# Kernel tuning notes

Measured on AMD Instinct MI355X. Metric: run time of the kernel, lower is better.

## Reference

```python
import jax, jax.numpy as jnp
import numpy as np

B, S, D = 2, 4096, 768
H = 12
HD = D // H  # 64


def setup_inputs() -> dict:
    key = jax.random.key(0)
    ks = jax.random.split(key, 6)
    scale = 0.02
    return {
        "x": jax.random.normal(ks[0], (B, S, D), dtype=jnp.float32),
        "w_query": jax.random.normal(ks[1], (D, D), dtype=jnp.float32) * scale,
        "w_key": jax.random.normal(ks[2], (D, D), dtype=jnp.float32) * scale,
        "w_value": jax.random.normal(ks[3], (D, D), dtype=jnp.float32) * scale,
        "w_out": jax.random.normal(ks[4], (D, D), dtype=jnp.float32) * scale,
        "b_out": jax.random.normal(ks[5], (D,), dtype=jnp.float32) * scale,
    }


def reference(x, w_query, w_key, w_value, w_out, b_out):
    b, s, d = x.shape
    # Linear(in, out) applies x @ W.T; weights here stored as [out, in]-equivalent
    # square matrices, so use x @ W.T for parity with torch semantics.
    q = (x @ w_query.T).reshape(b, s, H, HD).transpose(0, 2, 1, 3)  # [b,h,s,hd]
    k = (x @ w_key.T).reshape(b, s, H, HD).transpose(0, 2, 1, 3)
    v = (x @ w_value.T).reshape(b, s, H, HD).transpose(0, 2, 1, 3)

    scores = jnp.einsum("bhqd,bhkd->bhqk", q, k)  # [b,h,s,s]
    causal = jnp.triu(jnp.ones((s, s), dtype=bool), k=1)
    scores = jnp.where(causal, -jnp.inf, scores)
    # original scales AFTER masking: softmax(masked / sqrt(head_dim))
    att = jax.nn.softmax(scores / jnp.sqrt(jnp.float32(HD)), axis=-1)
    # dropout p=0.0 (eval) -> identity
    ctx = jnp.einsum("bhqk,bhkd->bhqd", att, v)  # [b,h,s,hd]
    ctx = ctx.transpose(0, 2, 1, 3).reshape(b, s, d)
    return ctx @ w_out.T + b_out
```

## Files before the change

### kernel.cpp

```cpp
#include <hip/hip_runtime.h>
#include <stdint.h>

typedef unsigned short u16;
typedef __attribute__((ext_vector_type(8))) short bf16x8;
typedef __attribute__((ext_vector_type(4))) float f32x4;

#define MFMA(a,b,c) __builtin_amdgcn_mfma_f32_16x16x32_bf16((a),(b),(c),0,0,0)

static constexpr int S  = 4096;
static constexpr int D  = 768;
static constexpr int H  = 12;
static constexpr int HD = 64;

__device__ __forceinline__ u16 f2b(float f){
  union { float f; unsigned u; } v; v.f = f;
  unsigned r = (v.u + 0x7fffu + ((v.u >> 16) & 1u)) >> 16;
  return (u16)r;
}

__device__ __forceinline__ unsigned pack_bf16_trunc(float a, float b){
  return __builtin_amdgcn_perm(__float_as_uint(b), __float_as_uint(a), 0x07060302u);
}

__device__ __forceinline__ void cp16(const u16* g, u16* l){
  __builtin_amdgcn_global_load_lds(
      (const __attribute__((address_space(1))) unsigned int*)g,
      (__attribute__((address_space(3))) unsigned int*)l, 16, 0, 0);
}

static constexpr int NX4 = (2 * S * D) / 4;
static constexpr int NW4 = (D * D) / 4;
__global__ void castall(const float* __restrict__ x,  const float* __restrict__ wq,
                        const float* __restrict__ wk, const float* __restrict__ wv,
                        const float* __restrict__ wo,
                        u16* __restrict__ xb,  u16* __restrict__ wqb,
                        u16* __restrict__ wkb, u16* __restrict__ wvb,
                        u16* __restrict__ wob){
  int i = blockIdx.x * 256 + threadIdx.x;
  const float* s; u16* d; int off;
  if (i < NX4) { s = x; d = xb; off = i; }
  else {
    int j = i - NX4; int wsel = j / NW4; off = j - wsel * NW4;
    if (wsel >= 4) return;
    s = (wsel == 0) ? wq : (wsel == 1) ? wk : (wsel == 2) ? wv : wo;
    d = (wsel == 0) ? wqb : (wsel == 1) ? wkb : (wsel == 2) ? wvb : wob;
  }
  float4 v = ((const float4*)s)[off];
  uint2 o;
  o.x = (unsigned)f2b(v.x) | ((unsigned)f2b(v.y) << 16);
  o.y = (unsigned)f2b(v.z) | ((unsigned)f2b(v.w) << 16);
  ((uint2*)d)[off] = o;
}

__global__ __launch_bounds__(256, 2) void qkv_gemm(
    const u16* __restrict__ xb, const u16* __restrict__ wq, const u16* __restrict__ wk,
    const u16* __restrict__ wv, u16* __restrict__ Qb, u16* __restrict__ Kb, u16* __restrict__ Vt)
{
  __shared__ __align__(16) u16 As[128 * 64];
  __shared__ __align__(16) u16 Bs[128 * 64];
  const int t = threadIdx.x;
  const int mblk = blockIdx.x, nblk = blockIdx.y, z = blockIdx.z;
  const u16* W = (z == 0) ? wq : (z == 1) ? wk : wv;
  const int w = t >> 6, lane = t & 63, quad = lane >> 4, l16 = lane & 15;
  const int wr = w >> 1, wc = w & 1;
  const int l7 = l16 & 7;

  f32x4 acc[4][4];
  #pragma unroll
  for (int i = 0; i < 4; i++)
    #pragma unroll
    for (int j = 0; j < 4; j++) acc[i][j] = (f32x4){0.f, 0.f, 0.f, 0.f};

  int srow[4], schk[4];
  #pragma unroll
  for (int i = 0; i < 4; i++) {
    int s = i * 256 + t;
    srow[i] = s >> 3;
    schk[i] = (s & 7) ^ (srow[i] & 7);
  }
  const u16* gA = xb + (size_t)(mblk * 128) * D;
  const u16* gB = W  + (size_t)(nblk * 128) * D;

  for (int k0 = 0; k0 < D; k0 += 64) {
    __syncthreads();
    #pragma unroll
    for (int i = 0; i < 4; i++) {
      int s = i * 256 + t;
      cp16(gA + (size_t)srow[i] * D + k0 + schk[i] * 8, As + s * 8);
      cp16(gB + (size_t)srow[i] * D + k0 + schk[i] * 8, Bs + s * 8);
    }
    __syncthreads();
    #pragma unroll
    for (int j = 0; j < 2; j++) {
      bf16x8 af[4], bfr[4];
      #pragma unroll
      for (int mt = 0; mt < 4; mt++)
        af[mt]  = *(const bf16x8*)(As + (wr * 64 + mt * 16 + l16) * 64 + ((j * 4 + quad) ^ l7) * 8);
      #pragma unroll
      for (int nt = 0; nt < 4; nt++)
        bfr[nt] = *(const bf16x8*)(Bs + (wc * 64 + nt * 16 + l16) * 64 + ((j * 4 + quad) ^ l7) * 8);
      #pragma unroll
      for (int mt = 0; mt < 4; mt++)
        #pragma unroll
        for (int nt = 0; nt < 4; nt++)
          acc[mt][nt] = MFMA(af[mt], bfr[nt], acc[mt][nt]);
    }
  }

  const float qscale = 0.18033688011112042f;
  #pragma unroll
  for (int mt = 0; mt < 4; mt++) {
    int m0 = mblk * 128 + wr * 64 + mt * 16 + quad * 4;
    #pragma unroll
    for (int nt = 0; nt < 4; nt++) {
      int n = nblk * 128 + wc * 64 + nt * 16 + l16;
      int h = n >> 6, hd = n & 63;
      if (z == 2) {
        int b = m0 >> 12, s0 = m0 & 4095;
        u16* p = Vt + (((size_t)(b * H + h) * HD + hd)) * S + s0;
        uint2 pk;
        pk.x = (unsigned)f2b(acc[mt][nt][0]) | ((unsigned)f2b(acc[mt][nt][1]) << 16);
        pk.y = (unsigned)f2b(acc[mt][nt][2]) | ((unsigned)f2b(acc[mt][nt][3]) << 16);
        *(uint2*)p = pk;
      } else {
        u16* dst = (z == 0) ? Qb : Kb;
        float sc = (z == 0) ? qscale : 1.0f;
        #pragma unroll
        for (int r = 0; r < 4; r++) {
          int m = m0 + r; int b = m >> 12, s = m & 4095;
          dst[((size_t)(b * H + h) * S + s) * HD + hd] = f2b(acc[mt][nt][r] * sc);
        }
      }
    }
  }
}

__global__ __launch_bounds__(256, 3) void attn(
    const u16* __restrict__ Qb, const u16* __restrict__ Kb,
    const u16* __restrict__ Vt, u16* __restrict__ ctx)
{
  __shared__ __align__(16) u16 Ks[128 * 64];
  __shared__ __align__(16) u16 Vts[64 * 128];
  __shared__ __align__(16) u16 Pb[4][32 * 72];
  const int t = threadIdx.x, w = t >> 6, lane = t & 63, quad = lane >> 4, l16 = lane & 15;
  const int l7 = l16 & 7;
  const int bh = blockIdx.x;
  const int qtile = 31 - (int)blockIdx.y;
  const int q0 = qtile * 128;
  const u16* Qh = Qb + (size_t)bh * S * HD;
  const u16* Kh = Kb + (size_t)bh * S * HD;
  const u16* Vh = Vt + (size_t)bh * S * HD;
  u16* Pw = &Pb[w][0];
  const int b = bh / H, h = bh % H;

  bf16x8 qf[2][2];
  #pragma unroll
  for (int rt = 0; rt < 2; rt++)
    #pragma unroll
    for (int ks = 0; ks < 2; ks++)
      qf[rt][ks] = *(const bf16x8*)(Qh + (size_t)(q0 + w * 32 + rt * 16 + l16) * HD + ks * 32 + quad * 8);

  f32x4 ao[2][4];
  #pragma unroll
  for (int rt = 0; rt < 2; rt++)
    #pragma unroll
    for (int co = 0; co < 4; co++) ao[rt][co] = (f32x4){0.f, 0.f, 0.f, 0.f};
  float lsum[2] = {0.f, 0.f};

  int krow[4], kchk[4], vrow[4], vchk[4];
  #pragma unroll
  for (int i = 0; i < 4; i++) {
    int s = i * 256 + t;
    krow[i] = s >> 3;  kchk[i] = (s & 7)  ^ (krow[i] & 7);
    vrow[i] = s >> 4;  vchk[i] = (s & 15) ^ (vrow[i] & 15);
  }

  for (int kv0 = 0; kv0 <= q0; kv0 += 128) {
    const bool diag = (kv0 == q0);
    const int ct_end = diag ? (2 * w + 2) : 8;
    const int ks_end = diag ? (w + 1) : 4;

    __syncthreads();
    #pragma unroll
    for (int i = 0; i < 4; i++) {
      int s = i * 256 + t;
      cp16(Kh + (size_t)(kv0 + krow[i]) * HD + kchk[i] * 8, Ks + s * 8);
      cp16(Vh + (size_t)vrow[i] * S + kv0 + vchk[i] * 8,    Vts + s * 8);
    }
    __syncthreads();

    #pragma unroll
    for (int h2 = 0; h2 < 2; h2++) {
      if (h2 * 4 < ct_end) {
        #pragma unroll
        for (int c2 = 0; c2 < 4; c2++) {
          int ct = h2 * 4 + c2;
          if (ct < ct_end) {
            int krw = ct * 16 + l16;
            bf16x8 kf0 = *(const bf16x8*)(Ks + krw * 64 + ((0 + quad) ^ l7) * 8);
            bf16x8 kf1 = *(const bf16x8*)(Ks + krw * 64 + ((4 + quad) ^ l7) * 8);
            f32x4 s0 = (f32x4){0.f, 0.f, 0.f, 0.f};
            f32x4 s1 = (f32x4){0.f, 0.f, 0.f, 0.f};
            s0 = MFMA(kf0, qf[0][0], s0);  s0 = MFMA(kf1, qf[0][1], s0);
            s1 = MFMA(kf0, qf[1][0], s1);  s1 = MFMA(kf1, qf[1][1], s1);
            if (diag) {
              int keyb = kv0 + ct * 16 + quad * 4;
              int qr0  = q0 + w * 32 + l16;
              #pragma unroll
              for (int r = 0; r < 4; r++) {
                if (keyb + r > qr0)      s0[r] = -1e30f;
                if (keyb + r > qr0 + 16) s1[r] = -1e30f;
              }
            }
            float p0 = __builtin_amdgcn_exp2f(s0[0]);
            float p1 = __builtin_amdgcn_exp2f(s0[1]);
            float p2 = __builtin_amdgcn_exp2f(s0[2]);
            float p3 = __builtin_amdgcn_exp2f(s0[3]);
            lsum[0] += (p0 + p1) + (p2 + p3);
            uint2 pk;
            pk.x = pack_bf16_trunc(p0, p1);
            pk.y = pack_bf16_trunc(p2, p3);
            *(uint2*)(Pw + l16 * 72 + c2 * 16 + quad * 4) = pk;
            p0 = __builtin_amdgcn_exp2f(s1[0]);
            p1 = __builtin_amdgcn_exp2f(s1[1]);
            p2 = __builtin_amdgcn_exp2f(s1[2]);
            p3 = __builtin_amdgcn_exp2f(s1[3]);
            lsum[1] += (p0 + p1) + (p2 + p3);
            pk.x = pack_bf16_trunc(p0, p1);
            pk.y = pack_bf16_trunc(p2, p3);
            *(uint2*)(Pw + (16 + l16) * 72 + c2 * 16 + quad * 4) = pk;
          }
        }
        #pragma unroll
        for (int k2 = 0; k2 < 2; k2++) {
          int ks = h2 * 2 + k2;
          if (ks < ks_end) {
            bf16x8 pf0 = *(const bf16x8*)(Pw + (0  + l16) * 72 + k2 * 32 + quad * 8);
            bf16x8 pf1 = *(const bf16x8*)(Pw + (16 + l16) * 72 + k2 * 32 + quad * 8);
            #pragma unroll
            for (int co = 0; co < 4; co++) {
              int vrw = co * 16 + l16;
              bf16x8 vf = *(const bf16x8*)(Vts + vrw * 128 + ((ks * 4 + quad) ^ (vrw & 15)) * 8);
              ao[0][co] = MFMA(vf, pf0, ao[0][co]);
              ao[1][co] = MFMA(vf, pf1, ao[1][co]);
            }
          }
        }
      }
    }
  }

  #pragma unroll
  for (int rt = 0; rt < 2; rt++) {
    float v = lsum[rt];
    v += __shfl_xor(v, 16, 64);
    v += __shfl_xor(v, 32, 64);
    float inv = 1.0f / v;
    int token = b * S + q0 + w * 32 + rt * 16 + l16;
    #pragma unroll
    for (int co = 0; co < 4; co++) {
      uint2 pk;
      pk.x = (unsigned)f2b(ao[rt][co][0] * inv) | ((unsigned)f2b(ao[rt][co][1] * inv) << 16);
      pk.y = (unsigned)f2b(ao[rt][co][2] * inv) | ((unsigned)f2b(ao[rt][co][3] * inv) << 16);
      *(uint2*)(ctx + (size_t)token * D + h * HD + co * 16 + quad * 4) = pk;
    }
  }
}

__global__ __launch_bounds__(256, 2) void out_gemm(
    const u16* __restrict__ ctx, const u16* __restrict__ wo,
    const float* __restrict__ bias, float* __restrict__ out)
{
  __shared__ __align__(16) u16 As[128 * 64];
  __shared__ __align__(16) u16 Bs[128 * 64];
  const int t = threadIdx.x;
  const int mblk = blockIdx.x, nblk = blockIdx.y;
  const int w = t >> 6, lane = t & 63, quad = lane >> 4, l16 = lane & 15;
  const int wr = w >> 1, wc = w & 1;
  const int l7 = l16 & 7;

  f32x4 acc[4][4];
  #pragma unroll
  for (int i = 0; i < 4; i++)
    #pragma unroll
    for (int j = 0; j < 4; j++) acc[i][j] = (f32x4){0.f, 0.f, 0.f, 0.f};

  int srow[4], schk[4];
  #pragma unroll
  for (int i = 0; i < 4; i++) {
    int s = i * 256 + t;
    srow[i] = s >> 3;
    schk[i] = (s & 7) ^ (srow[i] & 7);
  }
  const u16* gA = ctx + (size_t)(mblk * 128) * D;
  const u16* gB = wo  + (size_t)(nblk * 128) * D;

  for (int k0 = 0; k0 < D; k0 += 64) {
    __syncthreads();
    #pragma unroll
    for (int i = 0; i < 4; i++) {
      int s = i * 256 + t;
      cp16(gA + (size_t)srow[i] * D + k0 + schk[i] * 8, As + s * 8);
      cp16(gB + (size_t)srow[i] * D + k0 + schk[i] * 8, Bs + s * 8);
    }
    __syncthreads();
    #pragma unroll
    for (int j = 0; j < 2; j++) {
      bf16x8 af[4], bfr[4];
      #pragma unroll
      for (int mt = 0; mt < 4; mt++)
        af[mt]  = *(const bf16x8*)(As + (wr * 64 + mt * 16 + l16) * 64 + ((j * 4 + quad) ^ l7) * 8);
      #pragma unroll
      for (int nt = 0; nt < 4; nt++)
        bfr[nt] = *(const bf16x8*)(Bs + (wc * 64 + nt * 16 + l16) * 64 + ((j * 4 + quad) ^ l7) * 8);
      #pragma unroll
      for (int mt = 0; mt < 4; mt++)
        #pragma unroll
        for (int nt = 0; nt < 4; nt++)
          acc[mt][nt] = MFMA(af[mt], bfr[nt], acc[mt][nt]);
    }
  }

  #pragma unroll
  for (int mt = 0; mt < 4; mt++) {
    int m0 = mblk * 128 + wr * 64 + mt * 16 + quad * 4;
    #pragma unroll
    for (int nt = 0; nt < 4; nt++) {
      int n = nblk * 128 + wc * 64 + nt * 16 + l16;
      float bv = bias[n];
      #pragma unroll
      for (int r = 0; r < 4; r++)
        out[(size_t)(m0 + r) * D + n] = acc[mt][nt][r] + bv;
    }
  }
}

extern "C" void kernel_launch(void* const* d_in, const int* in_sizes, int n_in,
                              void* d_out, int out_size, void* d_ws, size_t ws_size,
                              hipStream_t stream) {
  const float* x    = (const float*)d_in[0];
  const float* wq   = (const float*)d_in[1];
  const float* wk   = (const float*)d_in[2];
  const float* wv   = (const float*)d_in[3];
  const float* wo   = (const float*)d_in[4];
  const float* bo   = (const float*)d_in[5];
  float* out = (float*)d_out;

  u16* ws = (u16*)d_ws;
  const size_t NX = (size_t)2 * S * D;
  const size_t NW = (size_t)D * D;
  u16* xb  = ws;
  u16* wqb = ws + NX;
  u16* wkb = wqb + NW;
  u16* wvb = wkb + NW;
  u16* wob = wvb + NW;
  u16* Qb  = wob + NW;
  u16* Kb  = Qb + NX;
  u16* Vt  = Kb + NX;
  u16* ctx = xb;

  const int total4 = NX4 + 4 * NW4;
  castall<<<(total4 + 255) / 256, 256, 0, stream>>>(x, wq, wk, wv, wo, xb, wqb, wkb, wvb, wob);

  qkv_gemm<<<dim3(64, 6, 3), 256, 0, stream>>>(xb, wqb, wkb, wvb, Qb, Kb, Vt);
  attn<<<dim3(24, 32), 256, 0, stream>>>(Qb, Kb, Vt, ctx);
  out_gemm<<<dim3(64, 6), 256, 0, stream>>>(ctx, wob, bo, out);
}
```

Measured before the change: 229.5 us.

## Split attention warps across key halves and transpose P in registers

Reorganizes the attention kernel so each wave owns 64 query rows and one half of the 128-key tile (2x2 wave grid). Partial outputs and row sums are then reduced through shared memory at the end. The P matrix no longer round-trips through an LDS buffer: it is rearranged into the MFMA operand layout with cross-lane shuffles. This is meant to remove LDS traffic and sync for P and to double K/V fragment reuse per wave. In exchange it costs more accumulator registers (16 f32x4), which may hurt occupancy at 3 blocks per SIMD, and it adds a final reduction. On the diagonal tile the causal work per wave is now uneven.

```diff
diff --git a/kernel.cpp b/kernel.cpp
--- a/kernel.cpp
+++ b/kernel.cpp
@@ -26,6 +26,30 @@
   __builtin_amdgcn_global_load_lds(
       (const __attribute__((address_space(1))) unsigned int*)g,
       (__attribute__((address_space(3))) unsigned int*)l, 16, 0, 0);
+}
+
+__device__ __forceinline__ bf16x8 quad_transpose(unsigned M0, unsigned M1,
+                                                 unsigned M2, unsigned M3, int quad){
+  const bool hi = (quad & 2) != 0;
+  unsigned e0 = hi ? M0 : M2;
+  unsigned e1 = hi ? M1 : M3;
+  unsigned f0 = (unsigned)__shfl_xor((int)e0, 32, 64);
+  unsigned f1 = (unsigned)__shfl_xor((int)e1, 32, 64);
+  unsigned A0 = hi ? f0 : M0;
+  unsigned A1 = hi ? f1 : M1;
+  unsigned A2 = hi ? M2 : f0;
+  unsigned A3 = hi ? M3 : f1;
+  const bool lo = (quad & 1) != 0;
+  e0 = lo ? A0 : A2;
+  e1 = lo ? A1 : A3;
+  f0 = (unsigned)__shfl_xor((int)e0, 16, 64);
+  f1 = (unsigned)__shfl_xor((int)e1, 16, 64);
+  union { unsigned u[4]; bf16x8 v; } r;
+  r.u[0] = lo ? f0 : A0;
+  r.u[1] = lo ? f1 : A1;
+  r.u[2] = lo ? A2 : f0;
+  r.u[3] = lo ? A3 : f1;
+  return r.v;
 }
 
 static constexpr int NX4 = (2 * S * D) / 4;
@@ -141,31 +165,31 @@
 {
   __shared__ __align__(16) u16 Ks[128 * 64];
   __shared__ __align__(16) u16 Vts[64 * 128];
-  __shared__ __align__(16) u16 Pb[4][32 * 72];
+  __shared__ float Lbuf[2][4][16];
   const int t = threadIdx.x, w = t >> 6, lane = t & 63, quad = lane >> 4, l16 = lane & 15;
   const int l7 = l16 & 7;
+  const int wq = w >> 1, wk = w & 1;
   const int bh = blockIdx.x;
   const int qtile = 31 - (int)blockIdx.y;
   const int q0 = qtile * 128;
   const u16* Qh = Qb + (size_t)bh * S * HD;
   const u16* Kh = Kb + (size_t)bh * S * HD;
   const u16* Vh = Vt + (size_t)bh * S * HD;
-  u16* Pw = &Pb[w][0];
   const int b = bh / H, h = bh % H;
 
-  bf16x8 qf[2][2];
-  #pragma unroll
-  for (int rt = 0; rt < 2; rt++)
-    #pragma unroll
-    for (int ks = 0; ks < 2; ks++)
-      qf[rt][ks] = *(const bf16x8*)(Qh + (size_t)(q0 + w * 32 + rt * 16 + l16) * HD + ks * 32 + quad * 8);
-
-  f32x4 ao[2][4];
-  #pragma unroll
-  for (int rt = 0; rt < 2; rt++)
-    #pragma unroll
-    for (int co = 0; co < 4; co++) ao[rt][co] = (f32x4){0.f, 0.f, 0.f, 0.f};
-  float lsum[2] = {0.f, 0.f};
+  bf16x8 qf[4][2];
+  #pragma unroll
+  for (int qt = 0; qt < 4; qt++)
+    #pragma unroll
+    for (int ksh = 0; ksh < 2; ksh++)
+      qf[qt][ksh] = *(const bf16x8*)(Qh + (size_t)(q0 + wq * 64 + qt * 16 + l16) * HD + ksh * 32 + quad * 8);
+
+  f32x4 ao[4][4];
+  #pragma unroll
+  for (int qt = 0; qt < 4; qt++)
+    #pragma unroll
+    for (int co = 0; co < 4; co++) ao[qt][co] = (f32x4){0.f, 0.f, 0.f, 0.f};
+  float lsum[4] = {0.f, 0.f, 0.f, 0.f};
 
   int krow[4], kchk[4], vrow[4], vchk[4];
   #pragma unroll
@@ -176,9 +200,9 @@
   }
 
   for (int kv0 = 0; kv0 <= q0; kv0 += 128) {
-    const bool diag = (kv0 == q0);
-    const int ct_end = diag ? (2 * w + 2) : 8;
-    const int ks_end = diag ? (w + 1) : 4;
+    const bool diag    = (kv0 == q0);
+    const bool skipall = diag && (wk > wq);
+    const bool mdiag   = diag && (wk == wq);
 
     __syncthreads();
     #pragma unroll
@@ -189,80 +213,89 @@
     }
     __syncthreads();
 
-    #pragma unroll
-    for (int h2 = 0; h2 < 2; h2++) {
-      if (h2 * 4 < ct_end) {
-        #pragma unroll
-        for (int c2 = 0; c2 < 4; c2++) {
-          int ct = h2 * 4 + c2;
-          if (ct < ct_end) {
-            int krw = ct * 16 + l16;
-            bf16x8 kf0 = *(const bf16x8*)(Ks + krw * 64 + ((0 + quad) ^ l7) * 8);
-            bf16x8 kf1 = *(const bf16x8*)(Ks + krw * 64 + ((4 + quad) ^ l7) * 8);
+    if (!skipall) {
+      #pragma unroll
+      for (int g = 0; g < 2; g++) {
+        unsigned pA[4][2], pB[4][2];
+        #pragma unroll
+        for (int ktL = 0; ktL < 2; ktL++) {
+          const int kt  = g * 2 + ktL;
+          const int krw = wk * 64 + kt * 16 + l16;
+          bf16x8 kf0 = *(const bf16x8*)(Ks + krw * 64 + ((0 + quad) ^ l7) * 8);
+          bf16x8 kf1 = *(const bf16x8*)(Ks + krw * 64 + ((4 + quad) ^ l7) * 8);
+          #pragma unroll
+          for (int qt = 0; qt < 4; qt++) {
             f32x4 s0 = (f32x4){0.f, 0.f, 0.f, 0.f};
-            f32x4 s1 = (f32x4){0.f, 0.f, 0.f, 0.f};
-            s0 = MFMA(kf0, qf[0][0], s0);  s0 = MFMA(kf1, qf[0][1], s0);
-            s1 = MFMA(kf0, qf[1][0], s1);  s1 = MFMA(kf1, qf[1][1], s1);
-            if (diag) {
-              int keyb = kv0 + ct * 16 + quad * 4;
-              int qr0  = q0 + w * 32 + l16;
+            s0 = MFMA(kf0, qf[qt][0], s0);
+            s0 = MFMA(kf1, qf[qt][1], s0);
+            if (mdiag) {
+              const int qoff = (qt - kt) * 16 + l16;
               #pragma unroll
-              for (int r = 0; r < 4; r++) {
-                if (keyb + r > qr0)      s0[r] = -1e30f;
-                if (keyb + r > qr0 + 16) s1[r] = -1e30f;
-              }
+              for (int r = 0; r < 4; r++)
+                s0[r] = (quad * 4 + r > qoff) ? -1e30f : s0[r];
             }
             float p0 = __builtin_amdgcn_exp2f(s0[0]);
             float p1 = __builtin_amdgcn_exp2f(s0[1]);
             float p2 = __builtin_amdgcn_exp2f(s0[2]);
             float p3 = __builtin_amdgcn_exp2f(s0[3]);
-            lsum[0] += (p0 + p1) + (p2 + p3);
-            uint2 pk;
-            pk.x = pack_bf16_trunc(p0, p1);
-            pk.y = pack_bf16_trunc(p2, p3);
-            *(uint2*)(Pw + l16 * 72 + c2 * 16 + quad * 4) = pk;
-            p0 = __builtin_amdgcn_exp2f(s1[0]);
-            p1 = __builtin_amdgcn_exp2f(s1[1]);
-            p2 = __builtin_amdgcn_exp2f(s1[2]);
-            p3 = __builtin_amdgcn_exp2f(s1[3]);
-            lsum[1] += (p0 + p1) + (p2 + p3);
-            pk.x = pack_bf16_trunc(p0, p1);
-            pk.y = pack_bf16_trunc(p2, p3);
-            *(uint2*)(Pw + (16 + l16) * 72 + c2 * 16 + quad * 4) = pk;
+            lsum[qt] += (p0 + p1) + (p2 + p3);
+            pA[qt][ktL] = pack_bf16_trunc(p0, p1);
+            pB[qt][ktL] = pack_bf16_trunc(p2, p3);
           }
         }
-        #pragma unroll
-        for (int k2 = 0; k2 < 2; k2++) {
-          int ks = h2 * 2 + k2;
-          if (ks < ks_end) {
-            bf16x8 pf0 = *(const bf16x8*)(Pw + (0  + l16) * 72 + k2 * 32 + quad * 8);
-            bf16x8 pf1 = *(const bf16x8*)(Pw + (16 + l16) * 72 + k2 * 32 + quad * 8);
-            #pragma unroll
-            for (int co = 0; co < 4; co++) {
-              int vrw = co * 16 + l16;
-              bf16x8 vf = *(const bf16x8*)(Vts + vrw * 128 + ((ks * 4 + quad) ^ (vrw & 15)) * 8);
-              ao[0][co] = MFMA(vf, pf0, ao[0][co]);
-              ao[1][co] = MFMA(vf, pf1, ao[1][co]);
-            }
-          }
+        bf16x8 pf[4];
+        #pragma unroll
+        for (int qt = 0; qt < 4; qt++)
+          pf[qt] = quad_transpose(pA[qt][0], pB[qt][0], pA[qt][1], pB[qt][1], quad);
+        #pragma unroll
+        for (int co = 0; co < 4; co++) {
+          const int vrw = co * 16 + l16;
+          bf16x8 vf = *(const bf16x8*)(Vts + vrw * 128 + ((wk * 8 + g * 4 + quad) ^ (vrw & 15)) * 8);
+          #pragma unroll
+          for (int qt = 0; qt < 4; qt++)
+            ao[qt][co] = MFMA(vf, pf[qt], ao[qt][co]);
         }
       }
     }
   }
 
   #pragma unroll
-  for (int rt = 0; rt < 2; rt++) {
-    float v = lsum[rt];
+  for (int qt = 0; qt < 4; qt++) {
+    float v = lsum[qt];
     v += __shfl_xor(v, 16, 64);
     v += __shfl_xor(v, 32, 64);
-    float inv = 1.0f / v;
-    int token = b * S + q0 + w * 32 + rt * 16 + l16;
-    #pragma unroll
-    for (int co = 0; co < 4; co++) {
-      uint2 pk;
-      pk.x = (unsigned)f2b(ao[rt][co][0] * inv) | ((unsigned)f2b(ao[rt][co][1] * inv) << 16);
-      pk.y = (unsigned)f2b(ao[rt][co][2] * inv) | ((unsigned)f2b(ao[rt][co][3] * inv) << 16);
-      *(uint2*)(ctx + (size_t)token * D + h * HD + co * 16 + quad * 4) = pk;
+    lsum[qt] = v;
+  }
+
+  __syncthreads();
+  float* red = wq ? (float*)Vts : (float*)Ks;
+  if (wk == 1) {
+    #pragma unroll
+    for (int qt = 0; qt < 4; qt++)
+      #pragma unroll
+      for (int co = 0; co < 4; co++)
+        *(f32x4*)(red + ((qt * 4 + co) * 64 + lane) * 4) = ao[qt][co];
+    if (lane < 16) {
+      #pragma unroll
+      for (int qt = 0; qt < 4; qt++) Lbuf[wq][qt][lane] = lsum[qt];
+    }
+  }
+  __syncthreads();
+  if (wk == 0) {
+    #pragma unroll
+    for (int qt = 0; qt < 4; qt++) {
+      float tot = lsum[qt] + Lbuf[wq][qt][l16];
+      float inv = 1.0f / tot;
+      int token = b * S + q0 + wq * 64 + qt * 16 + l16;
+      #pragma unroll
+      for (int co = 0; co < 4; co++) {
+        f32x4 pr = *(const f32x4*)(red + ((qt * 4 + co) * 64 + lane) * 4);
+        f32x4 sv = ao[qt][co] + pr;
+        uint2 pk;
+        pk.x = (unsigned)f2b(sv[0] * inv) | ((unsigned)f2b(sv[1] * inv) << 16);
+        pk.y = (unsigned)f2b(sv[2] * inv) | ((unsigned)f2b(sv[3] * inv) << 16);
+        *(uint2*)(ctx + (size_t)token * D + h * HD + co * 16 + quad * 4) = pk;
+      }
     }
   }
 }
```

Result: slower. 469.7 us (+104.7%).
